# Kernel tuning notes

Measured on AMD Instinct MI355X. Metric: run time of the kernel, lower is better.

Reference implementation:

```python
import jax, jax.numpy as jnp
import numpy as np
import math

D_MODEL, N_HEADS, D_K, D_V = 512, 2, 64, 64
C_CLIP = 10.0
MASK_FILL = -10.0

def setup_inputs() -> dict:
    key = jax.random.key(0)
    ks = jax.random.split(key, 12)
    B, Lq, Lk = 4, 2048, 2048
    s = 1.0 / math.sqrt(D_MODEL)
    return {
        "Q": jax.random.normal(ks[0], (B, Lq, D_MODEL), jnp.float32),
        "K": jax.random.normal(ks[1], (B, Lk, D_MODEL), jnp.float32),
        "V": jax.random.normal(ks[2], (B, Lk, D_MODEL), jnp.float32),
        "mask": jax.random.randint(ks[3], (B, Lk), 0, 2) > 0,
        "Wq": jax.random.normal(ks[4], (D_MODEL, N_HEADS * D_K), jnp.float32) * s,
        "bq": jnp.zeros((N_HEADS * D_K,), jnp.float32),
        "Wk": jax.random.normal(ks[5], (D_MODEL, N_HEADS * D_K), jnp.float32) * s,
        "bk": jnp.zeros((N_HEADS * D_K,), jnp.float32),
        "Wv": jax.random.normal(ks[6], (D_MODEL, N_HEADS * D_V), jnp.float32) * s,
        "bv": jnp.zeros((N_HEADS * D_V,), jnp.float32),
        "Wo": jax.random.normal(ks[7], (N_HEADS * D_V, D_MODEL), jnp.float32) * s,
        "bo": jnp.zeros((D_MODEL,), jnp.float32),
    }

def reference(Q, K, V, mask, Wq, bq, Wk, bk, Wv, bv, Wo, bo):
    B, Lq, _ = Q.shape
    Lk = K.shape[1]
    # project and split heads: [B, h, L, d]
    q = (Q @ Wq + bq).reshape(B, Lq, N_HEADS, D_K).transpose(0, 2, 1, 3)
    k = (K @ Wk + bk).reshape(B, Lk, N_HEADS, D_K).transpose(0, 2, 1, 3)
    v = (V @ Wv + bv).reshape(B, Lk, N_HEADS, D_V).transpose(0, 2, 1, 3)
    scores = jnp.einsum("bhqd,bhkd->bhqk", q, k) / jnp.sqrt(jnp.float32(D_K))
    scores = jnp.tanh(scores) * C_CLIP
    scores = jnp.where(mask[:, None, None, :], MASK_FILL, scores)
    attn = jax.nn.log_softmax(scores, axis=-1)  # NOTE: log-softmax used directly as weights
    out = jnp.einsum("bhqk,bhkd->bhqd", attn, v)
    out = out.transpose(0, 2, 1, 3).reshape(B, Lq, N_HEADS * D_V)
    out = out @ Wo + bo
    return (out, attn)
```

## Files before the change

### kernel.cpp

```cpp
#include <hip/hip_runtime.h>

typedef __attribute__((ext_vector_type(8))) short short8;
typedef __attribute__((ext_vector_type(4))) float f32x4;

#define DEVI static __device__ __forceinline__

constexpr int NB   = 4;
constexpr int NH   = 2;
constexpr int SEQ  = 2048;
constexpr int DM   = 512;
constexpr int DKV  = 64;
constexpr int HDIM = 128;

DEVI unsigned short f2bf(float f) {
    union { float f; unsigned u; } v; v.f = f;
    unsigned r = v.u + 0x7FFFu + ((v.u >> 16) & 1u);
    return (unsigned short)(r >> 16);
}
DEVI float bf2f(unsigned short s) {
    union { unsigned u; float f; } v; v.u = ((unsigned)s) << 16; return v.f;
}
DEVI void async16(const void* g, void* l) {
    __builtin_amdgcn_global_load_lds(
        (const __attribute__((address_space(1))) unsigned int*)g,
        (__attribute__((address_space(3))) unsigned int*)l, 16, 0, 0);
}

__global__ __launch_bounds__(256) void k_prep(
    const float* __restrict__ Wq, const float* __restrict__ Wk,
    const float* __restrict__ Wv, const float* __restrict__ Wo,
    unsigned short* __restrict__ Wqt, unsigned short* __restrict__ Wkt,
    unsigned short* __restrict__ Wvt, unsigned short* __restrict__ Wot) {
    int id = blockIdx.x * 256 + threadIdx.x;
    int which = id >> 16;
    int rem = id & 65535;
    if (which < 3) {
        const float* W = which == 0 ? Wq : (which == 1 ? Wk : Wv);
        unsigned short* Wt = which == 0 ? Wqt : (which == 1 ? Wkt : Wvt);
        int n = rem >> 9, k = rem & 511;
        Wt[rem] = f2bf(W[k * HDIM + n]);
    } else {
        int n = rem >> 7, k = rem & 127;
        Wot[rem] = f2bf(Wo[k * DM + n]);
    }
}

__global__ __launch_bounds__(256) void k_proj(
    const float* __restrict__ Qg, const float* __restrict__ Kg, const float* __restrict__ Vg,
    const unsigned short* __restrict__ Wqt, const unsigned short* __restrict__ Wkt,
    const unsigned short* __restrict__ Wvt,
    const float* __restrict__ bq, const float* __restrict__ bk, const float* __restrict__ bv,
    unsigned short* __restrict__ qs, unsigned short* __restrict__ kb,
    unsigned short* __restrict__ vt, float* __restrict__ colsumv) {
    __shared__ unsigned short lA[64 * 72];
    __shared__ unsigned short lB[128 * 64];

    const int y = blockIdx.y;
    const float* X = y == 0 ? Qg : (y == 1 ? Kg : Vg);
    const unsigned short* Wt = y == 0 ? Wqt : (y == 1 ? Wkt : Wvt);
    const float* bias = y == 0 ? bq : (y == 1 ? bk : bv);
    const float scal = y == 0 ? 0.125f : 1.0f;
    const int row0 = blockIdx.x * 64;
    const int tid = threadIdx.x, lane = tid & 63, wv = tid >> 6;
    const int l16 = lane & 15, lq4 = lane >> 4;
    const int wr = wv >> 1, wc = wv & 1;

    f32x4 acc[2][4];
    #pragma unroll
    for (int i = 0; i < 2; ++i)
        #pragma unroll
        for (int j = 0; j < 4; ++j) acc[i][j] = f32x4{0.f, 0.f, 0.f, 0.f};

    const int arow = tid >> 2, ac0 = (tid & 3) * 16;

    for (int kc = 0; kc < 8; ++kc) {
        {
            const float* src = X + (size_t)(row0 + arow) * DM + kc * 64 + ac0;
            unsigned short* dst = &lA[arow * 72 + ac0];
            #pragma unroll
            for (int i = 0; i < 4; ++i) {
                f32x4 v = __builtin_nontemporal_load((const f32x4*)(src + 4 * i));
                unsigned p0 = (unsigned)f2bf(v.x) | ((unsigned)f2bf(v.y) << 16);
                unsigned p1 = (unsigned)f2bf(v.z) | ((unsigned)f2bf(v.w) << 16);
                *(unsigned*)(dst + 4 * i) = p0;
                *(unsigned*)(dst + 4 * i + 2) = p1;
            }
        }
        #pragma unroll
        for (int c = 0; c < 4; ++c) {
            int chunk = wv * 4 + c;
            int flat = chunk * 64 + lane;
            int row = flat >> 3, cp = flat & 7, cc = cp ^ (row & 7);
            const void* g = (const char*)Wt + (size_t)row * 1024 + kc * 128 + cc * 16;
            void* l = (char*)lB + chunk * 1024 + lane * 16;
            async16(g, l);
        }
        __syncthreads();

        #pragma unroll
        for (int ks = 0; ks < 2; ++ks) {
            short8 a[2], b[4];
            #pragma unroll
            for (int mt = 0; mt < 2; ++mt) {
                int m = wr * 32 + mt * 16 + l16;
                a[mt] = *(const short8*)&lA[m * 72 + ks * 32 + lq4 * 8];
            }
            #pragma unroll
            for (int nt = 0; nt < 4; ++nt) {
                int n = wc * 64 + nt * 16 + l16;
                b[nt] = *(const short8*)&lB[n * 64 + (((ks * 4 + lq4) ^ (n & 7)) * 8)];
            }
            #pragma unroll
            for (int mt = 0; mt < 2; ++mt)
                #pragma unroll
                for (int nt = 0; nt < 4; ++nt)
                    acc[mt][nt] = __builtin_amdgcn_mfma_f32_16x16x32_bf16(
                        a[mt], b[nt], acc[mt][nt], 0, 0, 0);
        }
        __syncthreads();
    }

    if (y < 2) {
        unsigned short* dstp = (y == 0) ? qs : kb;
        #pragma unroll
        for (int mt = 0; mt < 2; ++mt)
            #pragma unroll
            for (int nt = 0; nt < 4; ++nt) {
                int col = wc * 64 + nt * 16 + l16;
                float bb = bias[col];
                int h = col >> 6, d = col & 63;
                #pragma unroll
                for (int r = 0; r < 4; ++r) {
                    int row = row0 + wr * 32 + mt * 16 + lq4 * 4 + r;
                    int b = row >> 11, pos = row & 2047;
                    float val = (acc[mt][nt][r] + bb) * scal;
                    dstp[((size_t)(b * NH + h) * SEQ + pos) * DKV + d] = f2bf(val);
                }
            }
    } else {
        #pragma unroll
        for (int mt = 0; mt < 2; ++mt)
            #pragma unroll
            for (int nt = 0; nt < 4; ++nt) {
                int col = wc * 64 + nt * 16 + l16;
                float bb = bias[col];
                #pragma unroll
                for (int r = 0; r < 4; ++r) {
                    int mrow = wr * 32 + mt * 16 + lq4 * 4 + r;
                    lB[col * 64 + mrow] = f2bf(acc[mt][nt][r] + bb);
                }
            }
        __syncthreads();
        {
            int c = tid >> 1, mp = (tid & 1) * 32;
            int b = row0 >> 11, kpos0 = row0 & 2047;
            int h = c >> 6, d = c & 63;
            unsigned short* dst = vt + ((size_t)(b * NH + h) * DKV + d) * SEQ + kpos0 + mp;
            const unsigned short* srcl = &lB[c * 64 + mp];
            #pragma unroll
            for (int i = 0; i < 4; ++i)
                *(uint4*)(dst + 8 * i) = *(const uint4*)(srcl + 8 * i);
        }
        {
            int col = tid >> 1, half = tid & 1;
            const unsigned short* p = &lB[col * 64 + half * 32];
            float s = 0.f;
            #pragma unroll
            for (int i = 0; i < 4; ++i) {
                short8 hv = *(const short8*)(p + 8 * i);
                #pragma unroll
                for (int j = 0; j < 8; ++j) s += bf2f((unsigned short)hv[j]);
            }
            s += __shfl_xor(s, 1);
            if (half == 0) {
                int ksp2 = (row0 & 2047) >> 9, bb = row0 >> 11;
                atomicAdd(&colsumv[((size_t)ksp2 * NB + bb) * HDIM + col], s);
            }
        }
    }
}

__global__ __launch_bounds__(256) void k_pass1(
    const unsigned short* __restrict__ qs, const unsigned short* __restrict__ kb,
    const int* __restrict__ maskg, unsigned short* __restrict__ sws,
    float* __restrict__ Lpart) {
    __shared__ unsigned short lK[128 * 64];
    __shared__ unsigned short lS[64 * 136];
    __shared__ int lM[128];
    __shared__ float lsumW[4 * 64];

    const int bx = blockIdx.x;
    const int ksp = bx & 3;
    const int qt = (bx >> 2) & 31;
    const int bh = bx >> 7;
    const int qbase = qt * 64;
    const int b = bh >> 1;
    const int tid = threadIdx.x, lane = tid & 63, wv = tid >> 6;
    const int l16 = lane & 15, lq4 = lane >> 4;

    short8 aq[4][2];
    #pragma unroll
    for (int mt = 0; mt < 4; ++mt)
        #pragma unroll
        for (int ks = 0; ks < 2; ++ks) {
            size_t off = ((size_t)bh * SEQ + qbase + mt * 16 + l16) * DKV + ks * 32 + lq4 * 8;
            aq[mt][ks] = *(const short8*)(qs + off);
        }

    float sums[4][4];
    #pragma unroll
    for (int mt = 0; mt < 4; ++mt)
        #pragma unroll
        for (int r = 0; r < 4; ++r) sums[mt][r] = 0.f;

    const char* kbase_ptr = (const char*)(kb + (size_t)bh * SEQ * DKV);

    for (int kt = ksp * 4; kt < ksp * 4 + 4; ++kt) {
        int kbase = kt * 128;
        #pragma unroll
        for (int c = 0; c < 4; ++c) {
            int chunk = wv * 4 + c;
            int flat = chunk * 64 + lane;
            int row = flat >> 3, cp = flat & 7, cc = cp ^ (row & 7);
            const void* g = kbase_ptr + (size_t)(kbase + row) * 128 + cc * 16;
            void* l = (char*)lK + chunk * 1024 + lane * 16;
            async16(g, l);
        }
        if (tid < 128) lM[tid] = maskg[b * SEQ + kbase + tid];
        __syncthreads();

        f32x4 acc[4][2];
        #pragma unroll
        for (int mt = 0; mt < 4; ++mt)
            #pragma unroll
            for (int nt = 0; nt < 2; ++nt) acc[mt][nt] = f32x4{0.f, 0.f, 0.f, 0.f};
        #pragma unroll
        for (int ks = 0; ks < 2; ++ks) {
            short8 bfr[2];
            #pragma unroll
            for (int nt = 0; nt < 2; ++nt) {
                int n = wv * 32 + nt * 16 + l16;
                bfr[nt] = *(const short8*)&lK[n * 64 + (((ks * 4 + lq4) ^ (n & 7)) * 8)];
            }
            #pragma unroll
            for (int mt = 0; mt < 4; ++mt)
                #pragma unroll
                for (int nt = 0; nt < 2; ++nt)
                    acc[mt][nt] = __builtin_amdgcn_mfma_f32_16x16x32_bf16(
                        aq[mt][ks], bfr[nt], acc[mt][nt], 0, 0, 0);
        }
        #pragma unroll
        for (int nt = 0; nt < 2; ++nt) {
            int col = wv * 32 + nt * 16 + l16;
            int mv = lM[col];
            #pragma unroll
            for (int mt = 0; mt < 4; ++mt)
                #pragma unroll
                for (int r = 0; r < 4; ++r) {
                    float x = acc[mt][nt][r];
                    float e2 = __expf(2.f * x);
                    float rr = __builtin_amdgcn_rcpf(1.f + e2);
                    rr = mv ? 1.f : rr;
                    float s10 = __builtin_fmaf(-20.f, rr, 10.f);
                    union { float f; unsigned u; } cv; cv.f = s10;
                    lS[(mt * 16 + lq4 * 4 + r) * 136 + col] = (unsigned short)(cv.u >> 16);
                    float t = __expf(-20.f * rr);
                    sums[mt][r] = __builtin_fmaf(22026.465795f, t, sums[mt][r]);
                }
        }
        __syncthreads();
        #pragma unroll
        for (int j = 0; j < 4; ++j) {
            int row = j * 16 + (tid >> 4);
            int coff = (tid & 15) * 8;
            uint4 dv = *(const uint4*)&lS[row * 136 + coff];
            *(uint4*)(sws + ((size_t)bh * SEQ + qbase + row) * SEQ + kbase + coff) = dv;
        }
    }

    #pragma unroll
    for (int mt = 0; mt < 4; ++mt)
        #pragma unroll
        for (int r = 0; r < 4; ++r) {
            float v = sums[mt][r];
            v += __shfl_xor(v, 1); v += __shfl_xor(v, 2);
            v += __shfl_xor(v, 4); v += __shfl_xor(v, 8);
            if (l16 == 0) lsumW[wv * 64 + mt * 16 + lq4 * 4 + r] = v;
        }
    __syncthreads();
    if (tid < 64) {
        float v = lsumW[tid] + lsumW[64 + tid] + lsumW[128 + tid] + lsumW[192 + tid];
        Lpart[(size_t)ksp * (8 * SEQ) + (size_t)bh * SEQ + qbase + tid] = v;
    }
}

__global__ __launch_bounds__(256) void k_pass2(
    const unsigned short* __restrict__ sws, const unsigned short* __restrict__ vt,
    const float* __restrict__ Lpart, const float* __restrict__ colsumv,
    float* __restrict__ attnG, float* __restrict__ outh2) {
    __shared__ unsigned short lV[64 * 128];
    __shared__ float lL[64];

    const int bx = blockIdx.x;
    const int ksp = bx & 3;
    const int qt = (bx >> 2) & 31;
    const int bh = bx >> 7;
    const int qbase = qt * 64;
    const int b = bh >> 1, h = bh & 1;
    const int tid = threadIdx.x, lane = tid & 63, wv = tid >> 6;
    const int l16 = lane & 15, lq4 = lane >> 4;

    if (tid < 64) {
        size_t idx = (size_t)bh * SEQ + qbase + tid;
        float s = Lpart[idx] + Lpart[8 * SEQ + idx] +
                  Lpart[2 * 8 * SEQ + idx] + Lpart[3 * 8 * SEQ + idx];
        lL[tid] = __logf(s);
    }
    __syncthreads();

    float Lr[4][4];
    #pragma unroll
    for (int mt = 0; mt < 4; ++mt)
        #pragma unroll
        for (int r = 0; r < 4; ++r) Lr[mt][r] = lL[mt * 16 + lq4 * 4 + r];

    f32x4 o[4];
    #pragma unroll
    for (int mt = 0; mt < 4; ++mt) o[mt] = f32x4{0.f, 0.f, 0.f, 0.f};

    const unsigned short* swsb = sws + (size_t)bh * SEQ * SEQ;

    for (int kti = 0; kti < 4; ++kti) {
        int kbase = ksp * 512 + kti * 128;
        #pragma unroll
        for (int c = 0; c < 4; ++c) {
            int chunk = wv * 4 + c;
            int flat = chunk * 64 + lane;
            int row = flat >> 4, cp = flat & 15, cc = cp ^ (row & 15);
            const void* g = (const char*)vt +
                (((size_t)bh * DKV + row) * SEQ + kbase) * 2 + cc * 16;
            void* l = (char*)lV + chunk * 1024 + lane * 16;
            async16(g, l);
        }
        __syncthreads();

        #pragma unroll
        for (int ks = 0; ks < 4; ++ks) {
            int d = wv * 16 + l16;
            short8 bfr = *(const short8*)&lV[d * 128 + (((ks * 4 + lq4) ^ (d & 15)) * 8)];
            #pragma unroll
            for (int mt = 0; mt < 4; ++mt) {
                const unsigned short* ap = swsb +
                    (size_t)(qbase + mt * 16 + l16) * SEQ + kbase + ks * 32 + lq4 * 8;
                short8 af = *(const short8*)ap;
                o[mt] = __builtin_amdgcn_mfma_f32_16x16x32_bf16(af, bfr, o[mt], 0, 0, 0);
            }
        }

        #pragma unroll
        for (int jr = 0; jr < 8; ++jr) {
            int row = jr * 8 + (tid >> 5);
            float Lv = lL[row];
            size_t roff = (size_t)(qbase + row) * SEQ + kbase + (tid & 31) * 4;
            uint2 w = *(const uint2*)(swsb + roff);
            union { unsigned u; float f; } t0, t1, t2, t3;
            t0.u = w.x << 16; t1.u = w.x & 0xFFFF0000u;
            t2.u = w.y << 16; t3.u = w.y & 0xFFFF0000u;
            f32x4 f;
            f.x = t0.f - Lv; f.y = t1.f - Lv; f.z = t2.f - Lv; f.w = t3.f - Lv;
            __builtin_nontemporal_store(f, (f32x4*)(attnG + (size_t)bh * SEQ * SEQ + roff));
        }
        __syncthreads();
    }

    int dcol = wv * 16 + l16;
    float csv = colsumv[((size_t)ksp * NB + b) * HDIM + h * DKV + dcol];
    float* dst = outh2 + (size_t)ksp * (8192 * HDIM);
    #pragma unroll
    for (int mt = 0; mt < 4; ++mt)
        #pragma unroll
        for (int r = 0; r < 4; ++r) {
            int q = qbase + mt * 16 + lq4 * 4 + r;
            float val = o[mt][r] - Lr[mt][r] * csv;
            dst[((size_t)b * SEQ + q) * HDIM + h * DKV + dcol] = val;
        }
}

__global__ __launch_bounds__(256) void k_oproj(
    const float* __restrict__ outh2, const unsigned short* __restrict__ Wot,
    const float* __restrict__ bo, float* __restrict__ outG) {
    __shared__ unsigned short lA2[128 * 128];
    __shared__ unsigned short lB2[128 * 128];
    const int row0 = blockIdx.x * 128, col0 = blockIdx.y * 128;
    const int tid = threadIdx.x, lane = tid & 63, wv = tid >> 6;
    const int l16 = lane & 15, lq4 = lane >> 4;
    const int wr = wv >> 1, wc = wv & 1;

    #pragma unroll
    for (int jj = 0; jj < 8; ++jj) {
        int flat = jj * 256 + tid;
        int row = flat >> 4, c = flat & 15;
        size_t gr = (size_t)(row0 + row) * HDIM + c * 8;
        float s[8];
        #pragma unroll
        for (int i = 0; i < 8; ++i) s[i] = 0.f;
        #pragma unroll
        for (int qq = 0; qq < 4; ++qq) {
            const float4* p = (const float4*)(outh2 + (size_t)qq * 1048576 + gr);
            float4 x0 = p[0], x1 = p[1];
            s[0] += x0.x; s[1] += x0.y; s[2] += x0.z; s[3] += x0.w;
            s[4] += x1.x; s[5] += x1.y; s[6] += x1.z; s[7] += x1.w;
        }
        unsigned d0 = (unsigned)f2bf(s[0]) | ((unsigned)f2bf(s[1]) << 16);
        unsigned d1 = (unsigned)f2bf(s[2]) | ((unsigned)f2bf(s[3]) << 16);
        unsigned d2 = (unsigned)f2bf(s[4]) | ((unsigned)f2bf(s[5]) << 16);
        unsigned d3 = (unsigned)f2bf(s[6]) | ((unsigned)f2bf(s[7]) << 16);
        uint4 pk; pk.x = d0; pk.y = d1; pk.z = d2; pk.w = d3;
        *(uint4*)&lA2[row * 128 + ((c ^ (row & 15)) * 8)] = pk;
    }
    #pragma unroll
    for (int c = 0; c < 8; ++c) {
        int chunk = wv * 8 + c;
        int flat = chunk * 64 + lane;
        int row = flat >> 4, cp = flat & 15, cc = cp ^ (row & 15);
        const void* g = (const char*)Wot + ((size_t)(col0 + row) * 128 + cc * 8) * 2;
        void* l = (char*)lB2 + chunk * 1024 + lane * 16;
        async16(g, l);
    }
    __syncthreads();

    f32x4 acc[4][4];
    #pragma unroll
    for (int mt = 0; mt < 4; ++mt)
        #pragma unroll
        for (int nt = 0; nt < 4; ++nt) acc[mt][nt] = f32x4{0.f, 0.f, 0.f, 0.f};

    #pragma unroll
    for (int ks = 0; ks < 4; ++ks) {
        short8 a[4], bfr[4];
        #pragma unroll
        for (int mt = 0; mt < 4; ++mt) {
            int row = wr * 64 + mt * 16 + l16;
            a[mt] = *(const short8*)&lA2[row * 128 + (((ks * 4 + lq4) ^ (row & 15)) * 8)];
        }
        #pragma unroll
        for (int nt = 0; nt < 4; ++nt) {
            int row = wc * 64 + nt * 16 + l16;
            bfr[nt] = *(const short8*)&lB2[row * 128 + (((ks * 4 + lq4) ^ (row & 15)) * 8)];
        }
        #pragma unroll
        for (int mt = 0; mt < 4; ++mt)
            #pragma unroll
            for (int nt = 0; nt < 4; ++nt)
                acc[mt][nt] = __builtin_amdgcn_mfma_f32_16x16x32_bf16(
                    a[mt], bfr[nt], acc[mt][nt], 0, 0, 0);
    }

    #pragma unroll
    for (int nt = 0; nt < 4; ++nt) {
        int col = col0 + wc * 64 + nt * 16 + l16;
        float bb = bo[col];
        #pragma unroll
        for (int mt = 0; mt < 4; ++mt)
            #pragma unroll
            for (int r = 0; r < 4; ++r) {
                int row = row0 + wr * 64 + mt * 16 + lq4 * 4 + r;
                outG[(size_t)row * DM + col] = acc[mt][nt][r] + bb;
            }
    }
}

extern "C" void kernel_launch(void* const* d_in, const int* in_sizes, int n_in,
                              void* d_out, int out_size, void* d_ws, size_t ws_size,
                              hipStream_t stream) {
    (void)in_sizes; (void)n_in; (void)out_size; (void)ws_size;
    const float* Qg = (const float*)d_in[0];
    const float* Kg = (const float*)d_in[1];
    const float* Vg = (const float*)d_in[2];
    const int*   maskg = (const int*)d_in[3];
    const float* Wq = (const float*)d_in[4];
    const float* bq = (const float*)d_in[5];
    const float* Wk = (const float*)d_in[6];
    const float* bk = (const float*)d_in[7];
    const float* Wv = (const float*)d_in[8];
    const float* bv = (const float*)d_in[9];
    const float* Wo = (const float*)d_in[10];
    const float* bo = (const float*)d_in[11];

    char* ws = (char*)d_ws;
    unsigned short* qs    = (unsigned short*)(ws);
    unsigned short* kb    = (unsigned short*)(ws + (4  << 20));
    unsigned short* vt    = (unsigned short*)(ws + (8  << 20));
    unsigned short* sws   = (unsigned short*)(ws + (12 << 20));
    float*          outh2 = (float*)(ws + (76 << 20));
    float*          Lpart = (float*)(ws + (92 << 20));
    float*          colsumv = (float*)(ws + (92 << 20) + 262144);
    unsigned short* Wqt   = (unsigned short*)(ws + (92 << 20) + 524288);
    unsigned short* Wkt   = (unsigned short*)((char*)Wqt + 131072);
    unsigned short* Wvt   = (unsigned short*)((char*)Wkt + 131072);
    unsigned short* Wot   = (unsigned short*)((char*)Wvt + 131072);

    float* outG  = (float*)d_out;
    float* attnG = outG + (size_t)NB * SEQ * DM;

    (void)hipMemsetAsync(colsumv, 0, 16 * HDIM * sizeof(float), stream);
    hipLaunchKernelGGL(k_prep, dim3(1024), dim3(256), 0, stream,
                       Wq, Wk, Wv, Wo, Wqt, Wkt, Wvt, Wot);
    hipLaunchKernelGGL(k_proj, dim3(128, 3), dim3(256), 0, stream,
                       Qg, Kg, Vg, Wqt, Wkt, Wvt, bq, bk, bv, qs, kb, vt, colsumv);
    hipLaunchKernelGGL(k_pass1, dim3(1024), dim3(256), 0, stream,
                       qs, kb, maskg, sws, Lpart);
    hipLaunchKernelGGL(k_pass2, dim3(1024), dim3(256), 0, stream,
                       sws, vt, Lpart, colsumv, attnG, outh2);
    hipLaunchKernelGGL(k_oproj, dim3(64, 4), dim3(256), 0, stream,
                       outh2, Wot, bo, outG);
}
```

Measured before the change: 289.0 us.

## Fuse attention passes into one kernel keeping score rows in LDS

The two attention kernels are merged into a single kernel that handles 16 query rows per block. It keeps the full 2048-wide bf16 score row in shared memory instead of writing it to and rereading it from a 64 MB global scratch buffer. The log-sum-exp is computed inside the block, so the cross-split partial sums and the partial-output reduction in the output projection go away, and the per-head output is stored as bf16. The cost is much less parallelism per block, serialized load-then-compute loops with full waitcnt stalls, and a large LDS footprint per block that limits occupancy.

```diff
diff --git a/kernel.cpp b/kernel.cpp
--- a/kernel.cpp
+++ b/kernel.cpp
@@ -11,6 +11,7 @@
 constexpr int DM   = 512;
 constexpr int DKV  = 64;
 constexpr int HDIM = 128;
+constexpr int ST   = 2050;
 
 DEVI unsigned short f2bf(float f) {
     union { float f; unsigned u; } v; v.f = f;
@@ -173,221 +174,159 @@
             }
             s += __shfl_xor(s, 1);
             if (half == 0) {
-                int ksp2 = (row0 & 2047) >> 9, bb = row0 >> 11;
-                atomicAdd(&colsumv[((size_t)ksp2 * NB + bb) * HDIM + col], s);
-            }
-        }
-    }
-}
-
-__global__ __launch_bounds__(256) void k_pass1(
+                int bb = row0 >> 11;
+                atomicAdd(&colsumv[(size_t)bb * HDIM + col], s);
+            }
+        }
+    }
+}
+
+__global__ __launch_bounds__(256, 2) void k_attn(
     const unsigned short* __restrict__ qs, const unsigned short* __restrict__ kb,
-    const int* __restrict__ maskg, unsigned short* __restrict__ sws,
-    float* __restrict__ Lpart) {
-    __shared__ unsigned short lK[128 * 64];
-    __shared__ unsigned short lS[64 * 136];
-    __shared__ int lM[128];
-    __shared__ float lsumW[4 * 64];
+    const unsigned short* __restrict__ vt, const int* __restrict__ maskg,
+    const float* __restrict__ colsumv, float* __restrict__ attnG,
+    unsigned short* __restrict__ outh) {
+    __shared__ unsigned short sArr[16 * ST];
+    __shared__ unsigned short stage[64 * 64];
+    __shared__ float lsumW[4 * 16];
+    __shared__ float lL[16];
 
     const int bx = blockIdx.x;
-    const int ksp = bx & 3;
-    const int qt = (bx >> 2) & 31;
-    const int bh = bx >> 7;
-    const int qbase = qt * 64;
-    const int b = bh >> 1;
-    const int tid = threadIdx.x, lane = tid & 63, wv = tid >> 6;
-    const int l16 = lane & 15, lq4 = lane >> 4;
-
-    short8 aq[4][2];
-    #pragma unroll
-    for (int mt = 0; mt < 4; ++mt)
-        #pragma unroll
-        for (int ks = 0; ks < 2; ++ks) {
-            size_t off = ((size_t)bh * SEQ + qbase + mt * 16 + l16) * DKV + ks * 32 + lq4 * 8;
-            aq[mt][ks] = *(const short8*)(qs + off);
-        }
-
-    float sums[4][4];
-    #pragma unroll
-    for (int mt = 0; mt < 4; ++mt)
-        #pragma unroll
-        for (int r = 0; r < 4; ++r) sums[mt][r] = 0.f;
-
-    const char* kbase_ptr = (const char*)(kb + (size_t)bh * SEQ * DKV);
-
-    for (int kt = ksp * 4; kt < ksp * 4 + 4; ++kt) {
-        int kbase = kt * 128;
-        #pragma unroll
-        for (int c = 0; c < 4; ++c) {
-            int chunk = wv * 4 + c;
-            int flat = chunk * 64 + lane;
-            int row = flat >> 3, cp = flat & 7, cc = cp ^ (row & 7);
-            const void* g = kbase_ptr + (size_t)(kbase + row) * 128 + cc * 16;
-            void* l = (char*)lK + chunk * 1024 + lane * 16;
-            async16(g, l);
-        }
-        if (tid < 128) lM[tid] = maskg[b * SEQ + kbase + tid];
-        __syncthreads();
-
-        f32x4 acc[4][2];
-        #pragma unroll
-        for (int mt = 0; mt < 4; ++mt)
-            #pragma unroll
-            for (int nt = 0; nt < 2; ++nt) acc[mt][nt] = f32x4{0.f, 0.f, 0.f, 0.f};
-        #pragma unroll
-        for (int ks = 0; ks < 2; ++ks) {
-            short8 bfr[2];
-            #pragma unroll
-            for (int nt = 0; nt < 2; ++nt) {
-                int n = wv * 32 + nt * 16 + l16;
-                bfr[nt] = *(const short8*)&lK[n * 64 + (((ks * 4 + lq4) ^ (n & 7)) * 8)];
-            }
-            #pragma unroll
-            for (int mt = 0; mt < 4; ++mt)
-                #pragma unroll
-                for (int nt = 0; nt < 2; ++nt)
-                    acc[mt][nt] = __builtin_amdgcn_mfma_f32_16x16x32_bf16(
-                        aq[mt][ks], bfr[nt], acc[mt][nt], 0, 0, 0);
-        }
-        #pragma unroll
-        for (int nt = 0; nt < 2; ++nt) {
-            int col = wv * 32 + nt * 16 + l16;
-            int mv = lM[col];
-            #pragma unroll
-            for (int mt = 0; mt < 4; ++mt)
-                #pragma unroll
-                for (int r = 0; r < 4; ++r) {
-                    float x = acc[mt][nt][r];
-                    float e2 = __expf(2.f * x);
-                    float rr = __builtin_amdgcn_rcpf(1.f + e2);
-                    rr = mv ? 1.f : rr;
-                    float s10 = __builtin_fmaf(-20.f, rr, 10.f);
-                    union { float f; unsigned u; } cv; cv.f = s10;
-                    lS[(mt * 16 + lq4 * 4 + r) * 136 + col] = (unsigned short)(cv.u >> 16);
-                    float t = __expf(-20.f * rr);
-                    sums[mt][r] = __builtin_fmaf(22026.465795f, t, sums[mt][r]);
-                }
-        }
-        __syncthreads();
-        #pragma unroll
-        for (int j = 0; j < 4; ++j) {
-            int row = j * 16 + (tid >> 4);
-            int coff = (tid & 15) * 8;
-            uint4 dv = *(const uint4*)&lS[row * 136 + coff];
-            *(uint4*)(sws + ((size_t)bh * SEQ + qbase + row) * SEQ + kbase + coff) = dv;
-        }
-    }
-
-    #pragma unroll
-    for (int mt = 0; mt < 4; ++mt)
-        #pragma unroll
-        for (int r = 0; r < 4; ++r) {
-            float v = sums[mt][r];
-            v += __shfl_xor(v, 1); v += __shfl_xor(v, 2);
-            v += __shfl_xor(v, 4); v += __shfl_xor(v, 8);
-            if (l16 == 0) lsumW[wv * 64 + mt * 16 + lq4 * 4 + r] = v;
-        }
-    __syncthreads();
-    if (tid < 64) {
-        float v = lsumW[tid] + lsumW[64 + tid] + lsumW[128 + tid] + lsumW[192 + tid];
-        Lpart[(size_t)ksp * (8 * SEQ) + (size_t)bh * SEQ + qbase + tid] = v;
-    }
-}
-
-__global__ __launch_bounds__(256) void k_pass2(
-    const unsigned short* __restrict__ sws, const unsigned short* __restrict__ vt,
-    const float* __restrict__ Lpart, const float* __restrict__ colsumv,
-    float* __restrict__ attnG, float* __restrict__ outh2) {
-    __shared__ unsigned short lV[64 * 128];
-    __shared__ float lL[64];
-
-    const int bx = blockIdx.x;
-    const int ksp = bx & 3;
-    const int qt = (bx >> 2) & 31;
-    const int bh = bx >> 7;
-    const int qbase = qt * 64;
+    const int bh = bx & 7;
+    const int qt = bx >> 3;
+    const int qbase = qt * 16;
     const int b = bh >> 1, h = bh & 1;
     const int tid = threadIdx.x, lane = tid & 63, wv = tid >> 6;
     const int l16 = lane & 15, lq4 = lane >> 4;
-
-    if (tid < 64) {
-        size_t idx = (size_t)bh * SEQ + qbase + tid;
-        float s = Lpart[idx] + Lpart[8 * SEQ + idx] +
-                  Lpart[2 * 8 * SEQ + idx] + Lpart[3 * 8 * SEQ + idx];
-        lL[tid] = __logf(s);
+    const int kcol = wv * 16 + l16;
+
+    short8 aq[2];
+    #pragma unroll
+    for (int ks = 0; ks < 2; ++ks)
+        aq[ks] = *(const short8*)(qs +
+            ((size_t)bh * SEQ + qbase + l16) * DKV + ks * 32 + lq4 * 8);
+
+    const char* kbb = (const char*)(kb + (size_t)bh * SEQ * DKV);
+    const char* vtb = (const char*)(vt + (size_t)bh * DKV * SEQ);
+
+    auto issueK = [&](int kt) {
+        int kbase = kt * 64;
+        #pragma unroll
+        for (int c = 0; c < 2; ++c) {
+            int chunk = wv * 2 + c;
+            int flat = chunk * 64 + lane;
+            int row = flat >> 3, cp = flat & 7, cc = cp ^ (row & 7);
+            async16(kbb + (size_t)(kbase + row) * 128 + cc * 16,
+                    (char*)stage + chunk * 1024 + lane * 16);
+        }
+    };
+    auto issueV = [&](int kt) {
+        int kbase = kt * 64;
+        #pragma unroll
+        for (int c = 0; c < 2; ++c) {
+            int chunk = wv * 2 + c;
+            int flat = chunk * 64 + lane;
+            int row = flat >> 3, cp = flat & 7, cc = cp ^ (row & 7);
+            async16(vtb + (size_t)row * (SEQ * 2) + kbase * 2 + cc * 16,
+                    (char*)stage + chunk * 1024 + lane * 16);
+        }
+    };
+
+    issueK(0);
+    int mv = maskg[b * SEQ + kcol];
+    float sums[4] = {0.f, 0.f, 0.f, 0.f};
+
+    for (int kt = 0; kt < 32; ++kt) {
+        int kbase = kt * 64;
+        asm volatile("s_waitcnt vmcnt(0)" ::: "memory");
+        short8 bfr[2];
+        #pragma unroll
+        for (int ks = 0; ks < 2; ++ks)
+            bfr[ks] = *(const short8*)&stage[kcol * 64 + (((ks * 4 + lq4) ^ (kcol & 7)) * 8)];
+        asm volatile("s_waitcnt lgkmcnt(0)" ::: "memory");
+        int mv_cur = mv;
+        if (kt < 31) {
+            issueK(kt + 1);
+            mv = maskg[b * SEQ + (kt + 1) * 64 + kcol];
+        }
+        f32x4 acc = {0.f, 0.f, 0.f, 0.f};
+        acc = __builtin_amdgcn_mfma_f32_16x16x32_bf16(aq[0], bfr[0], acc, 0, 0, 0);
+        acc = __builtin_amdgcn_mfma_f32_16x16x32_bf16(aq[1], bfr[1], acc, 0, 0, 0);
+        #pragma unroll
+        for (int r = 0; r < 4; ++r) {
+            float x = acc[r];
+            float e2 = __expf(2.f * x);
+            float rr = __builtin_amdgcn_rcpf(1.f + e2);
+            rr = mv_cur ? 1.f : rr;
+            float s10 = __builtin_fmaf(-20.f, rr, 10.f);
+            union { float f; unsigned u; } cv; cv.f = s10;
+            sArr[(lq4 * 4 + r) * ST + kbase + kcol] = (unsigned short)(cv.u >> 16);
+            float t = __expf(-20.f * rr);
+            sums[r] = __builtin_fmaf(22026.465795f, t, sums[r]);
+        }
+    }
+
+    #pragma unroll
+    for (int r = 0; r < 4; ++r) {
+        float v = sums[r];
+        v += __shfl_xor(v, 1); v += __shfl_xor(v, 2);
+        v += __shfl_xor(v, 4); v += __shfl_xor(v, 8);
+        if (l16 == 0) lsumW[wv * 16 + lq4 * 4 + r] = v;
     }
     __syncthreads();
-
-    float Lr[4][4];
-    #pragma unroll
-    for (int mt = 0; mt < 4; ++mt)
-        #pragma unroll
-        for (int r = 0; r < 4; ++r) Lr[mt][r] = lL[mt * 16 + lq4 * 4 + r];
-
-    f32x4 o[4];
-    #pragma unroll
-    for (int mt = 0; mt < 4; ++mt) o[mt] = f32x4{0.f, 0.f, 0.f, 0.f};
-
-    const unsigned short* swsb = sws + (size_t)bh * SEQ * SEQ;
-
-    for (int kti = 0; kti < 4; ++kti) {
-        int kbase = ksp * 512 + kti * 128;
-        #pragma unroll
-        for (int c = 0; c < 4; ++c) {
-            int chunk = wv * 4 + c;
-            int flat = chunk * 64 + lane;
-            int row = flat >> 4, cp = flat & 15, cc = cp ^ (row & 15);
-            const void* g = (const char*)vt +
-                (((size_t)bh * DKV + row) * SEQ + kbase) * 2 + cc * 16;
-            void* l = (char*)lV + chunk * 1024 + lane * 16;
-            async16(g, l);
-        }
-        __syncthreads();
-
-        #pragma unroll
-        for (int ks = 0; ks < 4; ++ks) {
-            int d = wv * 16 + l16;
-            short8 bfr = *(const short8*)&lV[d * 128 + (((ks * 4 + lq4) ^ (d & 15)) * 8)];
-            #pragma unroll
-            for (int mt = 0; mt < 4; ++mt) {
-                const unsigned short* ap = swsb +
-                    (size_t)(qbase + mt * 16 + l16) * SEQ + kbase + ks * 32 + lq4 * 8;
-                short8 af = *(const short8*)ap;
-                o[mt] = __builtin_amdgcn_mfma_f32_16x16x32_bf16(af, bfr, o[mt], 0, 0, 0);
-            }
-        }
-
-        #pragma unroll
-        for (int jr = 0; jr < 8; ++jr) {
-            int row = jr * 8 + (tid >> 5);
-            float Lv = lL[row];
-            size_t roff = (size_t)(qbase + row) * SEQ + kbase + (tid & 31) * 4;
-            uint2 w = *(const uint2*)(swsb + roff);
+    if (tid < 16)
+        lL[tid] = __logf(lsumW[tid] + lsumW[16 + tid] + lsumW[32 + tid] + lsumW[48 + tid]);
+    __syncthreads();
+
+    issueV(0);
+    f32x4 o = {0.f, 0.f, 0.f, 0.f};
+    for (int kt = 0; kt < 32; ++kt) {
+        int kbase = kt * 64;
+        asm volatile("s_waitcnt vmcnt(0)" ::: "memory");
+        short8 bfr[2], af[2];
+        #pragma unroll
+        for (int ks = 0; ks < 2; ++ks) {
+            bfr[ks] = *(const short8*)&stage[kcol * 64 + (((ks * 4 + lq4) ^ (kcol & 7)) * 8)];
+            af[ks]  = *(const short8*)&sArr[l16 * ST + kbase + ks * 32 + lq4 * 8];
+        }
+        asm volatile("s_waitcnt lgkmcnt(0)" ::: "memory");
+        if (kt < 31) issueV(kt + 1);
+        o = __builtin_amdgcn_mfma_f32_16x16x32_bf16(af[0], bfr[0], o, 0, 0, 0);
+        o = __builtin_amdgcn_mfma_f32_16x16x32_bf16(af[1], bfr[1], o, 0, 0, 0);
+    }
+
+    {
+        int wrow = tid >> 4, wj = tid & 15;
+        float Lv = lL[wrow];
+        const unsigned short* srow = &sArr[wrow * ST];
+        float* grow = attnG + ((size_t)bh * SEQ + qbase + wrow) * SEQ;
+        #pragma unroll 4
+        for (int i = 0; i < 32; ++i) {
+            int col = i * 64 + wj * 4;
+            uint2 w = *(const uint2*)(srow + col);
             union { unsigned u; float f; } t0, t1, t2, t3;
             t0.u = w.x << 16; t1.u = w.x & 0xFFFF0000u;
             t2.u = w.y << 16; t3.u = w.y & 0xFFFF0000u;
             f32x4 f;
             f.x = t0.f - Lv; f.y = t1.f - Lv; f.z = t2.f - Lv; f.w = t3.f - Lv;
-            __builtin_nontemporal_store(f, (f32x4*)(attnG + (size_t)bh * SEQ * SEQ + roff));
-        }
-        __syncthreads();
-    }
-
-    int dcol = wv * 16 + l16;
-    float csv = colsumv[((size_t)ksp * NB + b) * HDIM + h * DKV + dcol];
-    float* dst = outh2 + (size_t)ksp * (8192 * HDIM);
-    #pragma unroll
-    for (int mt = 0; mt < 4; ++mt)
+            __builtin_nontemporal_store(f, (f32x4*)(grow + col));
+        }
+    }
+
+    {
+        int d = wv * 16 + l16;
+        float csv = colsumv[(size_t)b * HDIM + h * DKV + d];
         #pragma unroll
         for (int r = 0; r < 4; ++r) {
-            int q = qbase + mt * 16 + lq4 * 4 + r;
-            float val = o[mt][r] - Lr[mt][r] * csv;
-            dst[((size_t)b * SEQ + q) * HDIM + h * DKV + dcol] = val;
-        }
+            int q = qbase + lq4 * 4 + r;
+            float val = o[r] - lL[lq4 * 4 + r] * csv;
+            outh[((size_t)b * SEQ + q) * HDIM + h * DKV + d] = f2bf(val);
+        }
+    }
 }
 
 __global__ __launch_bounds__(256) void k_oproj(
-    const float* __restrict__ outh2, const unsigned short* __restrict__ Wot,
+    const unsigned short* __restrict__ outh, const unsigned short* __restrict__ Wot,
     const float* __restrict__ bo, float* __restrict__ outG) {
     __shared__ unsigned short lA2[128 * 128];
     __shared__ unsigned short lB2[128 * 128];
@@ -397,26 +336,12 @@
     const int wr = wv >> 1, wc = wv & 1;
 
     #pragma unroll
-    for (int jj = 0; jj < 8; ++jj) {
-        int flat = jj * 256 + tid;
-        int row = flat >> 4, c = flat & 15;
-        size_t gr = (size_t)(row0 + row) * HDIM + c * 8;
-        float s[8];
-        #pragma unroll
-        for (int i = 0; i < 8; ++i) s[i] = 0.f;
-        #pragma unroll
-        for (int qq = 0; qq < 4; ++qq) {
-            const float4* p = (const float4*)(outh2 + (size_t)qq * 1048576 + gr);
-            float4 x0 = p[0], x1 = p[1];
-            s[0] += x0.x; s[1] += x0.y; s[2] += x0.z; s[3] += x0.w;
-            s[4] += x1.x; s[5] += x1.y; s[6] += x1.z; s[7] += x1.w;
-        }
-        unsigned d0 = (unsigned)f2bf(s[0]) | ((unsigned)f2bf(s[1]) << 16);
-        unsigned d1 = (unsigned)f2bf(s[2]) | ((unsigned)f2bf(s[3]) << 16);
-        unsigned d2 = (unsigned)f2bf(s[4]) | ((unsigned)f2bf(s[5]) << 16);
-        unsigned d3 = (unsigned)f2bf(s[6]) | ((unsigned)f2bf(s[7]) << 16);
-        uint4 pk; pk.x = d0; pk.y = d1; pk.z = d2; pk.w = d3;
-        *(uint4*)&lA2[row * 128 + ((c ^ (row & 15)) * 8)] = pk;
+    for (int c = 0; c < 8; ++c) {
+        int chunk = wv * 8 + c;
+        int flat = chunk * 64 + lane;
+        int row = flat >> 4, cp = flat & 15, cc = cp ^ (row & 15);
+        const void* g = (const char*)outh + (size_t)(row0 + row) * 256 + cc * 16;
+        async16(g, (char*)lA2 + chunk * 1024 + lane * 16);
     }
     #pragma unroll
     for (int c = 0; c < 8; ++c) {
@@ -424,8 +349,7 @@
         int flat = chunk * 64 + lane;
         int row = flat >> 4, cp = flat & 15, cc = cp ^ (row & 15);
         const void* g = (const char*)Wot + ((size_t)(col0 + row) * 128 + cc * 8) * 2;
-        void* l = (char*)lB2 + chunk * 1024 + lane * 16;
-        async16(g, l);
+        async16(g, (char*)lB2 + chunk * 1024 + lane * 16);
     }
     __syncthreads();
 
@@ -488,30 +412,26 @@
     const float* bo = (const float*)d_in[11];
 
     char* ws = (char*)d_ws;
-    unsigned short* qs    = (unsigned short*)(ws);
-    unsigned short* kb    = (unsigned short*)(ws + (4  << 20));
-    unsigned short* vt    = (unsigned short*)(ws + (8  << 20));
-    unsigned short* sws   = (unsigned short*)(ws + (12 << 20));
-    float*          outh2 = (float*)(ws + (76 << 20));
-    float*          Lpart = (float*)(ws + (92 << 20));
-    float*          colsumv = (float*)(ws + (92 << 20) + 262144);
-    unsigned short* Wqt   = (unsigned short*)(ws + (92 << 20) + 524288);
-    unsigned short* Wkt   = (unsigned short*)((char*)Wqt + 131072);
-    unsigned short* Wvt   = (unsigned short*)((char*)Wkt + 131072);
-    unsigned short* Wot   = (unsigned short*)((char*)Wvt + 131072);
+    unsigned short* qs      = (unsigned short*)(ws);
+    unsigned short* kb      = (unsigned short*)(ws + (4  << 20));
+    unsigned short* vt      = (unsigned short*)(ws + (8  << 20));
+    unsigned short* outh    = (unsigned short*)(ws + (12 << 20));
+    float*          colsumv = (float*)(ws + (14 << 20));
+    unsigned short* Wqt     = (unsigned short*)(ws + (14 << 20) + 8192);
+    unsigned short* Wkt     = (unsigned short*)((char*)Wqt + 131072);
+    unsigned short* Wvt     = (unsigned short*)((char*)Wkt + 131072);
+    unsigned short* Wot     = (unsigned short*)((char*)Wvt + 131072);
 
     float* outG  = (float*)d_out;
     float* attnG = outG + (size_t)NB * SEQ * DM;
 
-    (void)hipMemsetAsync(colsumv, 0, 16 * HDIM * sizeof(float), stream);
+    (void)hipMemsetAsync(colsumv, 0, NB * HDIM * sizeof(float), stream);
     hipLaunchKernelGGL(k_prep, dim3(1024), dim3(256), 0, stream,
                        Wq, Wk, Wv, Wo, Wqt, Wkt, Wvt, Wot);
     hipLaunchKernelGGL(k_proj, dim3(128, 3), dim3(256), 0, stream,
                        Qg, Kg, Vg, Wqt, Wkt, Wvt, bq, bk, bv, qs, kb, vt, colsumv);
-    hipLaunchKernelGGL(k_pass1, dim3(1024), dim3(256), 0, stream,
-                       qs, kb, maskg, sws, Lpart);
-    hipLaunchKernelGGL(k_pass2, dim3(1024), dim3(256), 0, stream,
-                       sws, vt, Lpart, colsumv, attnG, outh2);
+    hipLaunchKernelGGL(k_attn, dim3(1024), dim3(256), 0, stream,
+                       qs, kb, vt, maskg, colsumv, attnG, outh);
     hipLaunchKernelGGL(k_oproj, dim3(64, 4), dim3(256), 0, stream,
-                       outh2, Wot, bo, outG);
-}
+                       outh, Wot, bo, outG);
+}
```

Measured after the change: 269.0 us. 1.07x faster.
